# Kernel optimization log

Hardware: AMD Instinct MI355X
Metric: run time of the kernel (lower is better)

## Reference

```python
import jax, jax.numpy as jnp
import numpy as np

N_NODES = 100000
H_DIM = 128
N_RELS = 90   # num_rels*2 inside RGCN
N_BASES = 4
N_EDGES = 800000


def setup_inputs() -> dict:
    key = jax.random.key(0)
    k_emb, k_w, k_comp, k_r, k_norm, k_src, k_dst, k_b = jax.random.split(key, 8)
    h = jnp.arange(N_NODES, dtype=jnp.int64 if jax.config.jax_enable_x64 else jnp.int32)
    r = jax.random.randint(k_r, (N_EDGES,), 0, N_RELS)
    norm = jax.random.uniform(k_norm, (N_EDGES, 1), dtype=jnp.float32)
    src = jax.random.randint(k_src, (N_EDGES,), 0, N_NODES)
    dst = jax.random.randint(k_dst, (N_EDGES,), 0, N_NODES)
    # learned params (embedding table stands in for the word2vec-initialized table)
    emb_table = jax.random.normal(k_emb, (N_NODES, H_DIM), dtype=jnp.float32) * 0.02
    weight = jax.random.normal(k_w, (N_BASES, H_DIM, H_DIM), dtype=jnp.float32) * (1.0 / np.sqrt(H_DIM))
    w_comp = jax.random.normal(k_comp, (N_RELS, N_BASES), dtype=jnp.float32) * 0.5
    h_bias = jnp.zeros((H_DIM,), dtype=jnp.float32)
    return {"h": h, "r": r, "norm": norm, "src": src, "dst": dst,
            "emb_table": emb_table, "weight": weight, "w_comp": w_comp, "h_bias": h_bias}


def reference(h, r, norm, src, dst, emb_table, weight, w_comp, h_bias):
    # Input layer: embedding lookup on node ids  -> [N, D]
    x = emb_table[h]
    # Basis decomposition: project node feats onto each basis once  -> [N, B, D]
    # (avoids materializing per-edge [D,D] relation matrices)
    xb = jnp.einsum('ni,bio->nbo', x, weight)
    # Per-edge message: combine basis projections with relation coefficients
    coeff = w_comp[r]                       # [E, B]
    msg = jnp.einsum('ebo,eb->eo', xb[src], coeff)   # [E, D]
    msg = msg * norm                        # edge norm [E,1]
    # scatter-mean over destination nodes
    agg = jax.ops.segment_sum(msg, dst, num_segments=N_NODES)          # [N, D]
    cnt = jax.ops.segment_sum(jnp.ones((msg.shape[0],), msg.dtype), dst,
                              num_segments=N_NODES)                    # [N]
    node_repr = agg / jnp.maximum(cnt, 1.0)[:, None]
    # bias (RelGraphConv default bias=True); activation=None, self_loop=False, dropout=0
    node_repr = node_repr + h_bias
    return node_repr
```

## Files before the change

kernel.cpp:

```cpp
#include <hip/hip_runtime.h>
#include <hip/hip_bf16.h>

#define N_NODES 100000
#define H_DIM   128
#define N_RELS  90
#define N_BASES 4
#define N_EDGES 800000
#define SCAN_NB 391
#define NBLK    6250

typedef __attribute__((ext_vector_type(8))) __bf16 bf16x8;
typedef __attribute__((ext_vector_type(4))) float  floatx4;

#define WT_OFF     0
#define CNTS_OFF   131072
#define OFFS_OFF   531072
#define CURS_OFF   931072
#define BSUM_OFF   1331072
#define FLAG_OFF   1332672
#define RECS_OFF   1334272

__device__ __forceinline__ float bs2f(unsigned short s) {
    union { unsigned u; float f; } x; x.u = ((unsigned)s) << 16; return x.f;
}
__device__ __forceinline__ unsigned short f2bs(float f) {
    unsigned u = __float_as_uint(f);
    return (unsigned short)((u + 0x7fffu + ((u >> 16) & 1u)) >> 16);
}
__device__ __forceinline__ float ldf(const void* p, size_t i, int isbf) {
    return isbf ? bs2f(((const unsigned short*)p)[i]) : ((const float*)p)[i];
}
__device__ __forceinline__ int detect_bf(const void* norm) {
    const unsigned* w = (const unsigned*)norm;
    int hits = 0;
#pragma unroll
    for (int i = 0; i < 16; ++i) {
        unsigned b1 = (w[i] >> 8) & 0xffu;
        hits += (b1 >= 0x30u && b1 <= 0x3fu) ? 1 : 0;
    }
    return hits >= 12;
}

__global__ __launch_bounds__(256) void prep_count_k(const void* __restrict__ weight,
                                                    unsigned short* __restrict__ wt,
                                                    const int* __restrict__ dst,
                                                    int* __restrict__ counts,
                                                    const void* __restrict__ norm,
                                                    int* __restrict__ flag) {
    int b = blockIdx.x;
    if (b == 0 && threadIdx.x == 0) *flag = detect_bf(norm);
    if (b < 256) {
        int isbf = detect_bf(norm);
        int tid = b * 256 + threadIdx.x;
        int o = tid >> 9, c = tid & 511;
        int bb = c >> 7, i = c & 127;
        wt[tid] = f2bs(ldf(weight, (size_t)bb * 16384 + (size_t)i * 128 + o, isbf));
    } else {
        int e = (b - 256) * 256 + threadIdx.x;
        if (e < N_EDGES) atomicAdd(&counts[dst[e]], 1);
    }
}

__global__ __launch_bounds__(256) void scanA(const int* __restrict__ counts,
                                             int* __restrict__ offs, int* __restrict__ bsum) {
    __shared__ int s[256];
    int t = threadIdx.x, i = blockIdx.x * 256 + t;
    int v = (i < N_NODES) ? counts[i] : 0;
    s[t] = v; __syncthreads();
    for (int off = 1; off < 256; off <<= 1) {
        int x = (t >= off) ? s[t - off] : 0;
        __syncthreads(); s[t] += x; __syncthreads();
    }
    if (i < N_NODES) offs[i] = s[t] - v;
    if (t == 255) bsum[blockIdx.x] = s[255];
}

__global__ __launch_bounds__(256) void scanC2(int* __restrict__ offs,
                                              const int* __restrict__ bsum,
                                              int* __restrict__ cursor) {
    int b = blockIdx.x, t = threadIdx.x;
    int v = 0;
    if (t < b) v = bsum[t];
    if (t + 256 < b) v += bsum[t + 256];
    v += __shfl_down(v, 32); v += __shfl_down(v, 16);
    v += __shfl_down(v, 8);  v += __shfl_down(v, 4);
    v += __shfl_down(v, 2);  v += __shfl_down(v, 1);
    __shared__ int wsum[4];
    __shared__ int sprefix;
    if ((t & 63) == 0) wsum[t >> 6] = v;
    __syncthreads();
    if (t == 0) sprefix = wsum[0] + wsum[1] + wsum[2] + wsum[3];
    __syncthreads();
    int i = b * 256 + t;
    if (i < N_NODES) {
        int o = offs[i] + sprefix;
        offs[i] = o; cursor[i] = o;
    }
}

__global__ __launch_bounds__(256) void fill_k(const int* __restrict__ r, const void* __restrict__ norm,
                                              const int* __restrict__ src, const int* __restrict__ dst,
                                              const int* __restrict__ h,
                                              int* __restrict__ cursor,
                                              unsigned long long* __restrict__ recs) {
    int e = blockIdx.x * 256 + threadIdx.x;
    if (e >= N_EDGES) return;
    int isbf = detect_bf(norm);
    float nm = ldf(norm, e, isbf);
    unsigned lo = (unsigned)h[src[e]] | ((unsigned)r[e] << 20);
    unsigned long long rc = (unsigned long long)lo
                          | ((unsigned long long)__float_as_uint(nm) << 32);
    int pos = atomicAdd(&cursor[dst[e]], 1);
    __builtin_nontemporal_store(rc, &recs[pos]);
}

template <int ISBF>
__global__ __launch_bounds__(256) void fused_k(const int* __restrict__ counts,
                                               const int* __restrict__ offs,
                                               const unsigned long long* __restrict__ recs,
                                               const void* __restrict__ emb,
                                               const unsigned short* __restrict__ wt,
                                               const void* __restrict__ bias,
                                               const void* __restrict__ wcomp,
                                               const int* __restrict__ flag,
                                               void* __restrict__ out) {
    if ((*flag != 0) != (ISBF != 0)) return;
    __shared__ float wc[N_RELS * 4];
    __shared__ __align__(16) unsigned short y[16][520];
    for (int t = threadIdx.x; t < N_RELS * 4; t += 256) wc[t] = ldf(wcomp, t, ISBF);
    __syncthreads();

    int t = threadIdx.x;
    int lane = t & 63;
    int w = t >> 6;
    int g = lane >> 4, j = lane & 15;
    int blk = blockIdx.x;
    int dloc = w * 4 + g;
    int d = blk * 16 + dloc;
    int deg = counts[d], start = offs[d];
    float inv = 1.0f / (float)(deg > 1 ? deg : 1);

    float acc[4][8];
#pragma unroll
    for (int b = 0; b < 4; ++b)
#pragma unroll
        for (int c = 0; c < 8; ++c) acc[b][c] = 0.f;

    int kmax = __shfl(deg, 0);
    kmax = max(kmax, __shfl(deg, 16));
    kmax = max(kmax, __shfl(deg, 32));
    kmax = max(kmax, __shfl(deg, 48));

    unsigned long long rcur[4];
#pragma unroll
    for (int u = 0; u < 4; ++u)
        rcur[u] = __builtin_nontemporal_load(&recs[(u < deg) ? start + u : 0]);

    for (int k = 0; k < kmax; k += 4) {
        unsigned long long rnext[4];
#pragma unroll
        for (int u = 0; u < 4; ++u) {
            int kk = k + 4 + u;
            rnext[u] = __builtin_nontemporal_load(&recs[(kk < deg) ? start + kk : 0]);
        }
        bf16x8  rb[4];
        floatx4 rf[4][2];
        if (ISBF) {
#pragma unroll
            for (int u = 0; u < 4; ++u) {
                unsigned hx = (unsigned)rcur[u] & 0xFFFFFu;
                rb[u] = *(const bf16x8*)((const unsigned short*)emb + (size_t)hx * 128 + j * 8);
            }
        } else {
#pragma unroll
            for (int u = 0; u < 4; ++u) {
                unsigned hx = (unsigned)rcur[u] & 0xFFFFFu;
                const floatx4* f = (const floatx4*)((const float*)emb + (size_t)hx * 128 + j * 8);
                rf[u][0] = f[0]; rf[u][1] = f[1];
            }
        }
#pragma unroll
        for (int u = 0; u < 4; ++u) {
            bool v = (k + u) < deg;
            unsigned rel = ((unsigned)rcur[u] >> 20) & 0xFFFu;
            float nm = v ? __uint_as_float((unsigned)(rcur[u] >> 32)) : 0.f;
            const float* cw = &wc[rel * 4];
            float c0 = cw[0] * nm, c1 = cw[1] * nm, c2 = cw[2] * nm, c3 = cw[3] * nm;
            float x[8];
            if (ISBF) {
#pragma unroll
                for (int c = 0; c < 8; ++c) x[c] = (float)rb[u][c];
            } else {
#pragma unroll
                for (int c = 0; c < 4; ++c) { x[c] = rf[u][0][c]; x[c + 4] = rf[u][1][c]; }
            }
#pragma unroll
            for (int c = 0; c < 8; ++c) {
                acc[0][c] += c0 * x[c];
                acc[1][c] += c1 * x[c];
                acc[2][c] += c2 * x[c];
                acc[3][c] += c3 * x[c];
            }
        }
#pragma unroll
        for (int u = 0; u < 4; ++u) rcur[u] = rnext[u];
    }

#pragma unroll
    for (int b = 0; b < 4; ++b) {
        union { unsigned short u[8]; uint4 v; } pk;
#pragma unroll
        for (int c = 0; c < 8; ++c) pk.u[c] = f2bs(acc[b][c] * inv);
        *(uint4*)&y[dloc][b * 128 + j * 8] = pk.v;
    }
    __syncthreads();

    int m = lane & 15;
    int q = lane >> 4;
    for (int half = 0; half < 2; ++half) {
        int ct = w * 2 + half;
        floatx4 accm = {0.f, 0.f, 0.f, 0.f};
        const unsigned short* bp = wt + (size_t)(ct * 16 + m) * 512 + q * 8;
#pragma unroll
        for (int kc = 0; kc < 16; ++kc) {
            bf16x8 af = *(const bf16x8*)&y[m][kc * 32 + q * 8];
            bf16x8 bf = *(const bf16x8*)(bp + kc * 32);
            accm = __builtin_amdgcn_mfma_f32_16x16x32_bf16(af, bf, accm, 0, 0, 0);
        }
#pragma unroll
        for (int v = 0; v < 4; ++v) {
            int o = ct * 16 + m;
            float val = accm[v] + ldf(bias, o, ISBF);
            size_t oi = (size_t)(blk * 16 + q * 4 + v) * H_DIM + o;
            if (ISBF) __builtin_nontemporal_store(f2bs(val), (unsigned short*)out + oi);
            else      __builtin_nontemporal_store(val, (float*)out + oi);
        }
    }
}

extern "C" void kernel_launch(void* const* d_in, const int* in_sizes, int n_in,
                              void* d_out, int out_size, void* d_ws, size_t ws_size,
                              hipStream_t stream) {
    const int*  h      = (const int*)d_in[0];
    const int*  r      = (const int*)d_in[1];
    const void* norm   = d_in[2];
    const int*  src    = (const int*)d_in[3];
    const int*  dst    = (const int*)d_in[4];
    const void* emb    = d_in[5];
    const void* weight = d_in[6];
    const void* wcomp  = d_in[7];
    const void* bias   = d_in[8];

    char* ws = (char*)d_ws;
    unsigned short*     wt     = (unsigned short*)(ws + WT_OFF);
    int*                counts = (int*)(ws + CNTS_OFF);
    int*                offs   = (int*)(ws + OFFS_OFF);
    int*                cursor = (int*)(ws + CURS_OFF);
    int*                bsum   = (int*)(ws + BSUM_OFF);
    int*                flag   = (int*)(ws + FLAG_OFF);
    unsigned long long* recs   = (unsigned long long*)(ws + RECS_OFF);

    hipMemsetAsync(counts, 0, N_NODES * sizeof(int), stream);

    prep_count_k<<<256 + (N_EDGES + 255) / 256, 256, 0, stream>>>(weight, wt, dst, counts,
                                                                  norm, flag);
    scanA<<<SCAN_NB, 256, 0, stream>>>(counts, offs, bsum);
    scanC2<<<SCAN_NB, 256, 0, stream>>>(offs, bsum, cursor);
    fill_k<<<(N_EDGES + 255) / 256, 256, 0, stream>>>(r, norm, src, dst, h, cursor, recs);
    fused_k<1><<<NBLK, 256, 0, stream>>>(counts, offs, recs, emb, wt, bias, wcomp, flag, d_out);
    fused_k<0><<<NBLK, 256, 0, stream>>>(counts, offs, recs, emb, wt, bias, wcomp, flag, d_out);
}
```

Measured before the change: 338.8 us.

## Merge preprocessing kernels into one cooperative grid-synced kernel and drop dtype flag launch

Replaces the memset, counting, two scan kernels and fill kernel with a single cooperative kernel that uses grid syncs between phases. The dtype is now chosen on the host from the input size, so only one fused_k instantiation is launched instead of two with an early-exit flag. It also skips the h[src] gather when h is detected to be the identity, and uses normal stores instead of nontemporal ones. This removes several launch gaps, at the cost of grid-wide barriers and a fixed grid size for the atomic phases.

```diff
diff --git a/kernel.cpp b/kernel.cpp
--- a/kernel.cpp
+++ b/kernel.cpp
@@ -1,5 +1,8 @@
 #include <hip/hip_runtime.h>
 #include <hip/hip_bf16.h>
+#include <hip/hip_cooperative_groups.h>
+
+namespace cg = cooperative_groups;
 
 #define N_NODES 100000
 #define H_DIM   128
@@ -8,17 +11,18 @@
 #define N_EDGES 800000
 #define SCAN_NB 391
 #define NBLK    6250
+#define PREP_NB 1024
 
 typedef __attribute__((ext_vector_type(8))) __bf16 bf16x8;
 typedef __attribute__((ext_vector_type(4))) float  floatx4;
 
 #define WT_OFF     0
 #define CNTS_OFF   131072
-#define OFFS_OFF   531072
-#define CURS_OFF   931072
-#define BSUM_OFF   1331072
-#define FLAG_OFF   1332672
-#define RECS_OFF   1334272
+#define IDF_OFF    531072
+#define OFFS_OFF   531076
+#define CURS_OFF   931076
+#define BSUM_OFF   1331076
+#define RECS_OFF   1332640
 
 __device__ __forceinline__ float bs2f(unsigned short s) {
     union { unsigned u; float f; } x; x.u = ((unsigned)s) << 16; return x.f;
@@ -27,91 +31,96 @@
     unsigned u = __float_as_uint(f);
     return (unsigned short)((u + 0x7fffu + ((u >> 16) & 1u)) >> 16);
 }
-__device__ __forceinline__ float ldf(const void* p, size_t i, int isbf) {
-    return isbf ? bs2f(((const unsigned short*)p)[i]) : ((const float*)p)[i];
-}
-__device__ __forceinline__ int detect_bf(const void* norm) {
-    const unsigned* w = (const unsigned*)norm;
-    int hits = 0;
-#pragma unroll
-    for (int i = 0; i < 16; ++i) {
-        unsigned b1 = (w[i] >> 8) & 0xffu;
-        hits += (b1 >= 0x30u && b1 <= 0x3fu) ? 1 : 0;
-    }
-    return hits >= 12;
-}
-
-__global__ __launch_bounds__(256) void prep_count_k(const void* __restrict__ weight,
-                                                    unsigned short* __restrict__ wt,
-                                                    const int* __restrict__ dst,
-                                                    int* __restrict__ counts,
-                                                    const void* __restrict__ norm,
-                                                    int* __restrict__ flag) {
-    int b = blockIdx.x;
-    if (b == 0 && threadIdx.x == 0) *flag = detect_bf(norm);
-    if (b < 256) {
-        int isbf = detect_bf(norm);
-        int tid = b * 256 + threadIdx.x;
-        int o = tid >> 9, c = tid & 511;
-        int bb = c >> 7, i = c & 127;
-        wt[tid] = f2bs(ldf(weight, (size_t)bb * 16384 + (size_t)i * 128 + o, isbf));
-    } else {
-        int e = (b - 256) * 256 + threadIdx.x;
-        if (e < N_EDGES) atomicAdd(&counts[dst[e]], 1);
-    }
-}
-
-__global__ __launch_bounds__(256) void scanA(const int* __restrict__ counts,
-                                             int* __restrict__ offs, int* __restrict__ bsum) {
+template <int ISBF>
+__device__ __forceinline__ float ldT(const void* p, size_t i) {
+    if (ISBF) return bs2f(((const unsigned short*)p)[i]);
+    return ((const float*)p)[i];
+}
+
+template <int ISBF>
+__global__ __launch_bounds__(256) void prep_coop(const void* __restrict__ weight,
+                                                 unsigned short* __restrict__ wt,
+                                                 const int* __restrict__ dst,
+                                                 int* __restrict__ counts,
+                                                 const int* __restrict__ h,
+                                                 int* __restrict__ idflag,
+                                                 const int* __restrict__ r,
+                                                 const void* __restrict__ norm,
+                                                 const int* __restrict__ src,
+                                                 int* __restrict__ offs,
+                                                 int* __restrict__ cursor,
+                                                 int* __restrict__ bsum,
+                                                 unsigned long long* __restrict__ recs) {
+    cg::grid_group grid = cg::this_grid();
     __shared__ int s[256];
-    int t = threadIdx.x, i = blockIdx.x * 256 + t;
-    int v = (i < N_NODES) ? counts[i] : 0;
-    s[t] = v; __syncthreads();
-    for (int off = 1; off < 256; off <<= 1) {
-        int x = (t >= off) ? s[t - off] : 0;
-        __syncthreads(); s[t] += x; __syncthreads();
-    }
-    if (i < N_NODES) offs[i] = s[t] - v;
-    if (t == 255) bsum[blockIdx.x] = s[255];
-}
-
-__global__ __launch_bounds__(256) void scanC2(int* __restrict__ offs,
-                                              const int* __restrict__ bsum,
-                                              int* __restrict__ cursor) {
-    int b = blockIdx.x, t = threadIdx.x;
-    int v = 0;
-    if (t < b) v = bsum[t];
-    if (t + 256 < b) v += bsum[t + 256];
-    v += __shfl_down(v, 32); v += __shfl_down(v, 16);
-    v += __shfl_down(v, 8);  v += __shfl_down(v, 4);
-    v += __shfl_down(v, 2);  v += __shfl_down(v, 1);
     __shared__ int wsum[4];
-    __shared__ int sprefix;
-    if ((t & 63) == 0) wsum[t >> 6] = v;
+    __shared__ int sh_misc;
+
+    const int gtid = blockIdx.x * 256 + threadIdx.x;
+    const int gsz  = gridDim.x * 256;
+
+    for (int i = gtid; i <= N_NODES; i += gsz) atomicExch(&counts[i], 0);
+    for (int i = gtid; i < 65536; i += gsz) {
+        int o = i >> 9, c = i & 511, bb = c >> 7, ii = c & 127;
+        wt[i] = f2bs(ldT<ISBF>(weight, (size_t)bb * 16384 + (size_t)ii * 128 + o));
+    }
+    grid.sync();
+
+    for (int e = gtid; e < N_EDGES; e += gsz) atomicAdd(&counts[dst[e]], 1);
+    {
+        int bad = 0;
+        for (int i = gtid; i < N_NODES; i += gsz) bad |= (h[i] != i) ? 1 : 0;
+        if (bad) atomicOr(idflag, 1);
+    }
+    grid.sync();
+
+    if (blockIdx.x < SCAN_NB) {
+        int t = threadIdx.x, i = blockIdx.x * 256 + t;
+        int v = (i < N_NODES) ? atomicOr(&counts[i], 0) : 0;
+        s[t] = v; __syncthreads();
+        for (int off = 1; off < 256; off <<= 1) {
+            int x = (t >= off) ? s[t - off] : 0;
+            __syncthreads(); s[t] += x; __syncthreads();
+        }
+        if (i < N_NODES) offs[i] = s[t] - v;
+        if (t == 255) atomicExch(&bsum[blockIdx.x], s[255]);
+    }
+    grid.sync();
+
+    if (blockIdx.x < SCAN_NB) {
+        int b = blockIdx.x, t = threadIdx.x;
+        int v = 0;
+        if (t < b) v = atomicOr(&bsum[t], 0);
+        if (t + 256 < b) v += atomicOr(&bsum[t + 256], 0);
+        v += __shfl_down(v, 32); v += __shfl_down(v, 16);
+        v += __shfl_down(v, 8);  v += __shfl_down(v, 4);
+        v += __shfl_down(v, 2);  v += __shfl_down(v, 1);
+        if ((t & 63) == 0) wsum[t >> 6] = v;
+        __syncthreads();
+        if (t == 0) sh_misc = wsum[0] + wsum[1] + wsum[2] + wsum[3];
+        __syncthreads();
+        int i = b * 256 + t;
+        if (i < N_NODES) {
+            int o = offs[i] + sh_misc;
+            offs[i] = o;
+            atomicExch(&cursor[i], o);
+        }
+    }
+    grid.sync();
+
+    if (threadIdx.x == 0) sh_misc = atomicOr(idflag, 0);
     __syncthreads();
-    if (t == 0) sprefix = wsum[0] + wsum[1] + wsum[2] + wsum[3];
-    __syncthreads();
-    int i = b * 256 + t;
-    if (i < N_NODES) {
-        int o = offs[i] + sprefix;
-        offs[i] = o; cursor[i] = o;
-    }
-}
-
-__global__ __launch_bounds__(256) void fill_k(const int* __restrict__ r, const void* __restrict__ norm,
-                                              const int* __restrict__ src, const int* __restrict__ dst,
-                                              const int* __restrict__ h,
-                                              int* __restrict__ cursor,
-                                              unsigned long long* __restrict__ recs) {
-    int e = blockIdx.x * 256 + threadIdx.x;
-    if (e >= N_EDGES) return;
-    int isbf = detect_bf(norm);
-    float nm = ldf(norm, e, isbf);
-    unsigned lo = (unsigned)h[src[e]] | ((unsigned)r[e] << 20);
-    unsigned long long rc = (unsigned long long)lo
-                          | ((unsigned long long)__float_as_uint(nm) << 32);
-    int pos = atomicAdd(&cursor[dst[e]], 1);
-    __builtin_nontemporal_store(rc, &recs[pos]);
+    const int idf = sh_misc;
+    for (int e = gtid; e < N_EDGES; e += gsz) {
+        float nm = ldT<ISBF>(norm, e);
+        int sIdx = src[e];
+        int hs = idf ? h[sIdx] : sIdx;
+        unsigned lo = (unsigned)hs | ((unsigned)r[e] << 20);
+        unsigned long long rc = (unsigned long long)lo
+                              | ((unsigned long long)__float_as_uint(nm) << 32);
+        int pos = atomicAdd(&cursor[dst[e]], 1);
+        recs[pos] = rc;
+    }
 }
 
 template <int ISBF>
@@ -122,12 +131,10 @@
                                                const unsigned short* __restrict__ wt,
                                                const void* __restrict__ bias,
                                                const void* __restrict__ wcomp,
-                                               const int* __restrict__ flag,
                                                void* __restrict__ out) {
-    if ((*flag != 0) != (ISBF != 0)) return;
     __shared__ float wc[N_RELS * 4];
     __shared__ __align__(16) unsigned short y[16][520];
-    for (int t = threadIdx.x; t < N_RELS * 4; t += 256) wc[t] = ldf(wcomp, t, ISBF);
+    for (int t = threadIdx.x; t < N_RELS * 4; t += 256) wc[t] = ldT<ISBF>(wcomp, t);
     __syncthreads();
 
     int t = threadIdx.x;
@@ -230,12 +237,35 @@
 #pragma unroll
         for (int v = 0; v < 4; ++v) {
             int o = ct * 16 + m;
-            float val = accm[v] + ldf(bias, o, ISBF);
+            float val = accm[v] + ldT<ISBF>(bias, o);
             size_t oi = (size_t)(blk * 16 + q * 4 + v) * H_DIM + o;
-            if (ISBF) __builtin_nontemporal_store(f2bs(val), (unsigned short*)out + oi);
-            else      __builtin_nontemporal_store(val, (float*)out + oi);
-        }
-    }
+            if (ISBF) ((unsigned short*)out)[oi] = f2bs(val);
+            else      ((float*)out)[oi] = val;
+        }
+    }
+}
+
+template <int ISBF>
+static void launch_all(const int* h, const int* r, const void* norm, const int* src,
+                       const int* dst, const void* emb, const void* weight,
+                       const void* wcomp, const void* bias, char* ws, void* d_out,
+                       hipStream_t stream) {
+    unsigned short*     wt     = (unsigned short*)(ws + WT_OFF);
+    int*                counts = (int*)(ws + CNTS_OFF);
+    int*                idflag = (int*)(ws + IDF_OFF);
+    int*                offs   = (int*)(ws + OFFS_OFF);
+    int*                cursor = (int*)(ws + CURS_OFF);
+    int*                bsum   = (int*)(ws + BSUM_OFF);
+    unsigned long long* recs   = (unsigned long long*)(ws + RECS_OFF);
+
+    void* args[13] = { (void*)&weight, (void*)&wt, (void*)&dst, (void*)&counts,
+                       (void*)&h, (void*)&idflag, (void*)&r, (void*)&norm,
+                       (void*)&src, (void*)&offs, (void*)&cursor, (void*)&bsum,
+                       (void*)&recs };
+    hipLaunchCooperativeKernel(reinterpret_cast<void*>(&prep_coop<ISBF>),
+                               dim3(PREP_NB), dim3(256), args, 0, stream);
+
+    fused_k<ISBF><<<NBLK, 256, 0, stream>>>(counts, offs, recs, emb, wt, bias, wcomp, d_out);
 }
 
 extern "C" void kernel_launch(void* const* d_in, const int* in_sizes, int n_in,
@@ -250,23 +280,10 @@
     const void* weight = d_in[6];
     const void* wcomp  = d_in[7];
     const void* bias   = d_in[8];
-
     char* ws = (char*)d_ws;
-    unsigned short*     wt     = (unsigned short*)(ws + WT_OFF);
-    int*                counts = (int*)(ws + CNTS_OFF);
-    int*                offs   = (int*)(ws + OFFS_OFF);
-    int*                cursor = (int*)(ws + CURS_OFF);
-    int*                bsum   = (int*)(ws + BSUM_OFF);
-    int*                flag   = (int*)(ws + FLAG_OFF);
-    unsigned long long* recs   = (unsigned long long*)(ws + RECS_OFF);
-
-    hipMemsetAsync(counts, 0, N_NODES * sizeof(int), stream);
-
-    prep_count_k<<<256 + (N_EDGES + 255) / 256, 256, 0, stream>>>(weight, wt, dst, counts,
-                                                                  norm, flag);
-    scanA<<<SCAN_NB, 256, 0, stream>>>(counts, offs, bsum);
-    scanC2<<<SCAN_NB, 256, 0, stream>>>(offs, bsum, cursor);
-    fill_k<<<(N_EDGES + 255) / 256, 256, 0, stream>>>(r, norm, src, dst, h, cursor, recs);
-    fused_k<1><<<NBLK, 256, 0, stream>>>(counts, offs, recs, emb, wt, bias, wcomp, flag, d_out);
-    fused_k<0><<<NBLK, 256, 0, stream>>>(counts, offs, recs, emb, wt, bias, wcomp, flag, d_out);
-}
+
+    int isbf = (in_sizes[2] == (int)(N_EDGES * sizeof(unsigned short))) ? 1 : 0;
+
+    if (isbf) launch_all<1>(h, r, norm, src, dst, emb, weight, wcomp, bias, ws, d_out, stream);
+    else      launch_all<0>(h, r, norm, src, dst, emb, weight, wcomp, bias, ws, d_out, stream);
+}
```

Result: slower. 737.5 us (+117.7%).
